# Performance work log

Measured on AMD Instinct MI355X. Metric: run time of the kernel, lower is better.

The kernel has to match this reference:

```python
import jax, jax.numpy as jnp
import numpy as np

B, L, C, H, FF = 2, 2048, 1024, 16, 4096
HD = C // H
SCALE = HD ** -0.5
EPS = 1e-5


def _ln(x, g, b):
    m = jnp.mean(x, axis=-1, keepdims=True)
    v = jnp.mean((x - m) ** 2, axis=-1, keepdims=True)
    return (x - m) * jax.lax.rsqrt(v + EPS) * g + b


def setup_inputs() -> dict:
    key = jax.random.key(0)
    ks = jax.random.split(key, 12)
    s = lambda fan_in: 1.0 / np.sqrt(fan_in)
    return {
        "x": jax.random.normal(ks[0], (B, L, C), jnp.float32),
        "freq_diff": jax.random.normal(ks[1], (B, L), jnp.float32),
        "qkv_w": jax.random.normal(ks[2], (C, 3 * C), jnp.float32) * s(C),
        "qkv_b": jnp.zeros((3 * C,), jnp.float32),
        "fp_w1": jax.random.normal(ks[3], (1, C), jnp.float32),
        "fp_b1": jnp.zeros((C,), jnp.float32),
        "fp_ln_g": jnp.ones((C,), jnp.float32),
        "fp_ln_b": jnp.zeros((C,), jnp.float32),
        "fp_w2": jax.random.normal(ks[4], (C, C), jnp.float32) * s(C),
        "fp_b2": jnp.zeros((C,), jnp.float32),
        "wq_w": jax.random.normal(ks[5], (HD, HD), jnp.float32) * s(HD),
        "wq_b": jnp.zeros((HD,), jnp.float32),
        "wk_w": jax.random.normal(ks[6], (HD, HD), jnp.float32) * s(HD),
        "wk_b": jnp.zeros((HD,), jnp.float32),
        "out_w": jax.random.normal(ks[7], (C, C), jnp.float32) * s(C),
        "out_b": jnp.zeros((C,), jnp.float32),
        "n1_g": jnp.ones((C,), jnp.float32),
        "n1_b": jnp.zeros((C,), jnp.float32),
        "n2_g": jnp.ones((C,), jnp.float32),
        "n2_b": jnp.zeros((C,), jnp.float32),
        "mlp_w1": jax.random.normal(ks[8], (C, FF), jnp.float32) * s(C),
        "mlp_b1": jnp.zeros((FF,), jnp.float32),
        "mlp_w2": jax.random.normal(ks[9], (FF, C), jnp.float32) * s(FF),
        "mlp_b2": jnp.zeros((C,), jnp.float32),
        "freq_scale": jnp.ones((1,), jnp.float32),
    }


def reference(x, freq_diff, qkv_w, qkv_b, fp_w1, fp_b1, fp_ln_g, fp_ln_b,
              fp_w2, fp_b2, wq_w, wq_b, wk_w, wk_b, out_w, out_b,
              n1_g, n1_b, n2_g, n2_b, mlp_w1, mlp_b1, mlp_w2, mlp_b2,
              freq_scale):
    shortcut = x
    xn = _ln(x, n1_g, n1_b)
    qkv = (xn @ qkv_w + qkv_b).reshape(B, L, 3, H, HD)
    qkv = jnp.transpose(qkv, (2, 0, 3, 1, 4))  # [3,B,H,L,HD]
    q, k, v = qkv[0], qkv[1], qkv[2]

    # frequency bias: MLP on scalar freq_diff -> per-head bias vectors
    fb = freq_diff[..., None] @ fp_w1 + fp_b1          # [B,L,C]
    fb = jax.nn.gelu(_ln(fb, fp_ln_g, fp_ln_b), approximate=False)
    fb = fb @ fp_w2 + fp_b2                            # [B,L,C]
    fb = jnp.transpose(fb.reshape(B, L, H, HD), (0, 2, 1, 3))  # [B,H,L,HD]
    qb = fb @ wq_w + wq_b
    kb = fb @ wk_w + wk_b
    freq_attn_bias = jnp.einsum('bhqd,bhkd->bhqk', qb, kb)

    attn = jnp.einsum('bhqd,bhkd->bhqk', q, k) * SCALE
    attn = attn + freq_scale[0] * freq_attn_bias
    attn = jax.nn.softmax(attn, axis=-1)
    o = jnp.einsum('bhqk,bhkd->bhqd', attn, v)
    o = jnp.transpose(o, (0, 2, 1, 3)).reshape(B, L, C)
    x = shortcut + (o @ out_w + out_b)

    xn2 = _ln(x, n2_g, n2_b)
    h = jax.nn.gelu(xn2 @ mlp_w1 + mlp_b1, approximate=False)
    x = x + (h @ mlp_w2 + mlp_b2)
    return x
```

## Files before the change

### kernel.cpp

```cpp
#include <hip/hip_runtime.h>
#include <math.h>


typedef __bf16 bf16;
typedef float f32x4 __attribute__((ext_vector_type(4)));
typedef bf16 bf16x8 __attribute__((ext_vector_type(8)));
typedef bf16 bf16x4 __attribute__((ext_vector_type(4)));

#define DEVINL __device__ __forceinline__

#define LOG2E 1.4426950408889634f

DEVINL float fast_exp2(float x) { return __builtin_amdgcn_exp2f(x); }

DEVINL void async_load16(const void* g, void* l) {
  __builtin_amdgcn_global_load_lds(
      (const __attribute__((address_space(1))) unsigned int*)g,
      (__attribute__((address_space(3))) unsigned int*)l, 16, 0, 0);
}

DEVINL f32x4 mfma16(bf16x8 a, bf16x8 b, f32x4 c) {
  return __builtin_amdgcn_mfma_f32_16x16x32_bf16(a, b, c, 0, 0, 0);
}

DEVINL float gelu_exact(float v) {
  return 0.5f * v * (1.0f + erff(v * 0.70710678118654752f));
}

DEVINL void hard_barrier() {
  asm volatile("" ::: "memory");
  __builtin_amdgcn_s_barrier();
  asm volatile("" ::: "memory");
}

DEVINL void block_reduce2(float& a, float& b, float* red, int tid) {
#pragma unroll
  for (int off = 32; off >= 1; off >>= 1) {
    a += __shfl_xor(a, off);
    b += __shfl_xor(b, off);
  }
  int w = tid >> 6;
  if ((tid & 63) == 0) { red[2 * w] = a; red[2 * w + 1] = b; }
  __syncthreads();
  a = red[0] + red[2] + red[4] + red[6];
  b = red[1] + red[3] + red[5] + red[7];
  __syncthreads();
}

__global__ __launch_bounds__(256) void pre_kernel(
    const float* __restrict__ qkv_w, const float* __restrict__ out_w,
    const float* __restrict__ mlp_w1, const float* __restrict__ mlp_w2,
    bf16* __restrict__ qkv_wt, bf16* __restrict__ out_wt,
    bf16* __restrict__ w1t, bf16* __restrict__ w2t,
    const float* __restrict__ x, const float* __restrict__ fd,
    const float* __restrict__ g1, const float* __restrict__ b1,
    const float* __restrict__ fw1, const float* __restrict__ fb1,
    const float* __restrict__ flg, const float* __restrict__ flb,
    bf16* __restrict__ xn, bf16* __restrict__ gout) {
  __shared__ float tile[32][33];
  __shared__ float red[8];
  const int id = blockIdx.x, t = threadIdx.x;
  if (id < 12288) {
    const float* W; bf16* Wt; int K, N, bx, by;
    if (id < 3072) {
      W = qkv_w; Wt = qkv_wt; K = 1024; N = 3072; bx = id % 96; by = id / 96;
    } else if (id < 4096) {
      int i = id - 3072;
      W = out_w; Wt = out_wt; K = 1024; N = 1024; bx = i & 31; by = i >> 5;
    } else if (id < 8192) {
      int i = id - 4096;
      W = mlp_w1; Wt = w1t; K = 1024; N = 4096; bx = i & 127; by = i >> 7;
    } else {
      int i = id - 8192;
      W = mlp_w2; Wt = w2t; K = 4096; N = 1024; bx = i & 31; by = i >> 5;
    }
    int n0 = bx * 32, k0 = by * 32;
    int tx = t & 31, ty = t >> 5;
#pragma unroll
    for (int r = 0; r < 4; ++r)
      tile[ty + r * 8][tx] = W[(size_t)(k0 + ty + r * 8) * N + n0 + tx];
    __syncthreads();
#pragma unroll
    for (int r = 0; r < 4; ++r)
      Wt[(size_t)(n0 + ty + r * 8) * K + k0 + tx] = (bf16)tile[tx][ty + r * 8];
    return;
  }
  int tok = id - 12288;
  float4 xv = ((const float4*)(x + (size_t)tok * 1024))[t];
  float s = xv.x + xv.y + xv.z + xv.w;
  float ss = xv.x * xv.x + xv.y * xv.y + xv.z * xv.z + xv.w * xv.w;
  block_reduce2(s, ss, red, t);
  float mean = s * (1.0f / 1024.0f);
  float rsig = rsqrtf(ss * (1.0f / 1024.0f) - mean * mean + 1e-5f);
  float4 g4 = ((const float4*)g1)[t], b4 = ((const float4*)b1)[t];
  bf16x4 o;
  o[0] = (bf16)((xv.x - mean) * rsig * g4.x + b4.x);
  o[1] = (bf16)((xv.y - mean) * rsig * g4.y + b4.y);
  o[2] = (bf16)((xv.z - mean) * rsig * g4.z + b4.z);
  o[3] = (bf16)((xv.w - mean) * rsig * g4.w + b4.w);
  ((bf16x4*)xn)[(size_t)tok * 256 + t] = o;

  float dv = fd[tok];
  float4 w4 = ((const float4*)fw1)[t], c4 = ((const float4*)fb1)[t];
  float f0 = dv * w4.x + c4.x, f1 = dv * w4.y + c4.y;
  float f2 = dv * w4.z + c4.z, f3 = dv * w4.w + c4.w;
  s = f0 + f1 + f2 + f3;
  ss = f0 * f0 + f1 * f1 + f2 * f2 + f3 * f3;
  block_reduce2(s, ss, red, t);
  mean = s * (1.0f / 1024.0f);
  rsig = rsqrtf(ss * (1.0f / 1024.0f) - mean * mean + 1e-5f);
  float4 lg = ((const float4*)flg)[t], lb = ((const float4*)flb)[t];
  bf16x4 q;
  q[0] = (bf16)gelu_exact((f0 - mean) * rsig * lg.x + lb.x);
  q[1] = (bf16)gelu_exact((f1 - mean) * rsig * lg.y + lb.y);
  q[2] = (bf16)gelu_exact((f2 - mean) * rsig * lg.z + lb.z);
  q[3] = (bf16)gelu_exact((f3 - mean) * rsig * lg.w + lb.w);
  ((bf16x4*)gout)[(size_t)tok * 256 + t] = q;
}

__global__ __launch_bounds__(256) void prec_qk(
    const float* __restrict__ fp_w2, const float* __restrict__ fp_b2,
    const float* __restrict__ wq_w, const float* __restrict__ wq_b,
    const float* __restrict__ wk_w, const float* __restrict__ wk_b,
    bf16* __restrict__ wqk2t, float* __restrict__ bqk) {
  __shared__ float Wl[64 * 64];
  __shared__ float Al[64 * 128];
  const int id = blockIdx.x;
  const int sel = id >> 7, h = (id >> 3) & 15, ck = id & 7;
  const int t = threadIdx.x;
  const float* wsel = sel ? wk_w : wq_w;
#pragma unroll
  for (int i = 0; i < 4; ++i)
    ((float4*)Wl)[i * 256 + t] = ((const float4*)wsel)[i * 256 + t];
  const int c0 = ck * 128, off = h * 64;
#pragma unroll
  for (int it = 0; it < 8; ++it) {
    int idx = it * 256 + t;
    int rr = idx >> 4, c4 = idx & 15;
    float4 v = *(const float4*)(fp_w2 + (size_t)(c0 + rr) * 1024 + off + c4 * 4);
    float vv[4] = {v.x, v.y, v.z, v.w};
#pragma unroll
    for (int k = 0; k < 4; ++k) {
      int i2 = c4 * 4 + k;
      Al[i2 * 128 + (rr ^ (i2 & 31))] = vv[k];
    }
  }
  __syncthreads();
  const int cr = t & 127, jh = (t >> 7) * 32;
  float acc[32];
#pragma unroll
  for (int j = 0; j < 32; ++j) acc[j] = 0.f;
  for (int i = 0; i < 64; ++i) {
    float a = Al[i * 128 + (cr ^ (i & 31))];
    const float4* wrow = (const float4*)(Wl + i * 64 + jh);
#pragma unroll
    for (int j4 = 0; j4 < 8; ++j4) {
      float4 wv = wrow[j4];
      acc[j4 * 4 + 0] += a * wv.x;
      acc[j4 * 4 + 1] += a * wv.y;
      acc[j4 * 4 + 2] += a * wv.z;
      acc[j4 * 4 + 3] += a * wv.w;
    }
  }
  const int nbase = sel * 1024 + off + jh;
#pragma unroll
  for (int j = 0; j < 32; ++j)
    wqk2t[(size_t)(nbase + j) * 1024 + c0 + cr] = (bf16)acc[j];
  if (ck == 0 && t < 64) {
    float s = 0.f;
    for (int i = 0; i < 64; ++i) s += fp_b2[off + i] * Wl[i * 64 + t];
    bqk[sel * 1024 + off + t] = s + (sel ? wk_b[t] : wq_b[t]);
  }
}

__global__ __launch_bounds__(256) void reduce_oln(
    const float* __restrict__ part, const float* __restrict__ x,
    const float* __restrict__ outb, const float* __restrict__ b2,
    const float* __restrict__ g, const float* __restrict__ bb,
    float* __restrict__ out0, bf16* __restrict__ ln2) {
  __shared__ float red[8];
  int tok = blockIdx.x, t = threadIdx.x;
  size_t base = (size_t)tok * 256 + t;
  const size_t S = (size_t)4096 * 256;
  float4 p0 = ((const float4*)part)[base];
  float4 p1 = ((const float4*)part)[base + S];
  float4 xv = ((const float4*)x)[base];
  float4 ob = ((const float4*)outb)[t];
  float v0 = xv.x + p0.x + p1.x + ob.x;
  float v1 = xv.y + p0.y + p1.y + ob.y;
  float v2 = xv.z + p0.z + p1.z + ob.z;
  float v3 = xv.w + p0.w + p1.w + ob.w;
  float s = v0 + v1 + v2 + v3;
  float ss = v0 * v0 + v1 * v1 + v2 * v2 + v3 * v3;
  block_reduce2(s, ss, red, t);
  float mean = s * (1.0f / 1024.0f);
  float rsig = rsqrtf(ss * (1.0f / 1024.0f) - mean * mean + 1e-5f);
  float4 g4 = ((const float4*)g)[t], bb4 = ((const float4*)bb)[t];
  bf16x4 o;
  o[0] = (bf16)((v0 - mean) * rsig * g4.x + bb4.x);
  o[1] = (bf16)((v1 - mean) * rsig * g4.y + bb4.y);
  o[2] = (bf16)((v2 - mean) * rsig * g4.z + bb4.z);
  o[3] = (bf16)((v3 - mean) * rsig * g4.w + bb4.w);
  ((bf16x4*)ln2)[base] = o;
  float4 b24 = ((const float4*)b2)[t];
  float4 ov;
  ov.x = v0 + b24.x; ov.y = v1 + b24.y; ov.z = v2 + b24.z; ov.w = v3 + b24.w;
  ((float4*)out0)[base] = ov;
}

#define PHASE(MH, NH, LA, LB, STAGE_STMT, WAIT_STMT)                          \
  do {                                                                        \
    if (LA) {                                                                 \
      _Pragma("unroll") for (int ml = 0; ml < 4; ++ml) {                      \
        _Pragma("unroll") for (int ks = 0; ks < 2; ++ks) {                    \
          const int rr = ml * 16 + lm;                                        \
          const int cc = (((ks * 4 + quad) ^ (lm & 7)) << 3);                 \
          af[ml][ks] = *(const bf16x8*)&As[bsel][MH][wm][rr][cc];             \
        }                                                                     \
      }                                                                       \
    }                                                                         \
    if (LB) {                                                                 \
      _Pragma("unroll") for (int nl = 0; nl < 2; ++nl) {                      \
        _Pragma("unroll") for (int ks = 0; ks < 2; ++ks) {                    \
          const int rr = nl * 16 + lm;                                        \
          const int cc = (((ks * 4 + quad) ^ (lm & 7)) << 3);                 \
          bfr[nl][ks] = *(const bf16x8*)&Bs[bsel][NH][wn][rr][cc];            \
        }                                                                     \
      }                                                                       \
    }                                                                         \
    STAGE_STMT;                                                               \
    WAIT_STMT;                                                                \
    hard_barrier();                                                           \
    __builtin_amdgcn_s_setprio(1);                                            \
    _Pragma("unroll") for (int ks = 0; ks < 2; ++ks) {                        \
      _Pragma("unroll") for (int ml = 0; ml < 4; ++ml) {                      \
        _Pragma("unroll") for (int nl = 0; nl < 2; ++nl) {                    \
          acc[(MH)*4 + ml][(NH)*2 + nl] = mfma16(                             \
              af[ml][ks], bfr[nl][ks], acc[(MH)*4 + ml][(NH)*2 + nl]);        \
        }                                                                     \
      }                                                                       \
    }                                                                         \
    __builtin_amdgcn_s_setprio(0);                                            \
  } while (0)

template <class Epi>
__global__ __launch_bounds__(512, 2) void gemm256(
    const bf16* __restrict__ A, const bf16* __restrict__ Bt,
    int lda, int ldb, int K, int kstride, int nbx, int nblk, int rowoffz,
    Epi epi) {
  __shared__ __align__(16) bf16 As[2][2][2][64][64];
  __shared__ __align__(16) bf16 Bs[2][2][4][32][64];

  const int tid = threadIdx.x;
  const int lane = tid & 63, w = tid >> 6;
  const int quad = lane >> 4, lm = lane & 15;
  const int wm = w >> 2, wn = w & 3;

  const int kz = blockIdx.x / nblk;
  const int bid = blockIdx.x - kz * nblk;
  const int swz = (nblk & 7) ? bid : ((bid & 7) * (nblk >> 3) + (bid >> 3));
  const int tm = swz / nbx, tn = swz - tm * nbx;
  const int m0 = tm << 8, n0 = tn << 8;
  const int rowoff = kz * rowoffz;
  A += (size_t)kz * kstride;
  Bt += (size_t)kz * kstride;

  const bf16* Abase = A + (size_t)m0 * lda;
  const bf16* Bbase = Bt + (size_t)n0 * ldb;

  auto stageA = [&](int b, int mh, int kt) {
#pragma unroll
    for (int j = 0; j < 2; ++j) {
      const int q = (w * 2 + j) * 64 + lane;
      const int wm2 = q >> 9, rr = (q >> 3) & 63, c = q & 7;
      async_load16(Abase + (size_t)(wm2 * 128 + mh * 64 + rr) * lda +
                       (size_t)kt * 64 + ((c ^ (rr & 7)) << 3),
                   (char*)&As[b][mh][0][0][0] + (w * 2 + j) * 1024);
    }
  };
  auto stageB = [&](int b, int nh, int kt) {
#pragma unroll
    for (int j = 0; j < 2; ++j) {
      const int q = (w * 2 + j) * 64 + lane;
      const int wn4 = q >> 8, rr = (q >> 3) & 31, c = q & 7;
      async_load16(Bbase + (size_t)(wn4 * 64 + nh * 32 + rr) * ldb +
                       (size_t)kt * 64 + ((c ^ (rr & 7)) << 3),
                   (char*)&Bs[b][nh][0][0][0] + (w * 2 + j) * 1024);
    }
  };

  f32x4 acc[8][4];
#pragma unroll
  for (int i = 0; i < 8; ++i)
#pragma unroll
    for (int j = 0; j < 4; ++j) {
      acc[i][j][0] = 0.f; acc[i][j][1] = 0.f;
      acc[i][j][2] = 0.f; acc[i][j][3] = 0.f;
    }
  bf16x8 af[4][2], bfr[2][2];

  stageA(0, 0, 0);
  stageB(0, 1, 0);
  stageA(0, 1, 0);
  stageB(0, 0, 0);
  stageA(1, 0, 1);
  stageB(1, 1, 1);
  asm volatile("s_waitcnt vmcnt(4)" ::: "memory");
  hard_barrier();

  const int nt = K >> 6;
  int bsel = 0;
  for (int t = 0; t < nt; ++t, bsel ^= 1) {
    PHASE(0, 0, 1, 1, { if (t + 1 < nt) stageA(bsel ^ 1, 1, t + 1); }, {});
    PHASE(0, 1, 0, 1, { if (t + 1 < nt) stageB(bsel ^ 1, 0, t + 1); }, {});
    PHASE(1, 1, 1, 0, { if (t + 2 < nt) stageA(bsel, 0, t + 2); }, {});
    PHASE(1, 0, 0, 1, { if (t + 2 < nt) stageB(bsel, 1, t + 2); },
          {
            if (t + 2 < nt) {
              asm volatile("s_waitcnt vmcnt(4)" ::: "memory");
            } else if (t + 1 < nt) {
              asm volatile("s_waitcnt vmcnt(0)" ::: "memory");
            }
          });
  }

#pragma unroll
  for (int mi = 0; mi < 8; ++mi)
#pragma unroll
    for (int ni = 0; ni < 4; ++ni)
      epi(rowoff + m0 + wm * 128 + mi * 16 + quad * 4,
          n0 + wn * 64 + ni * 16 + lm, acc[mi][ni]);
}

__global__ __launch_bounds__(256) void reduce_mlp2(
    const float* __restrict__ part, float* __restrict__ out) {
  size_t i = (size_t)blockIdx.x * 256 + threadIdx.x;
  const float4* p = (const float4*)part;
  float4 o = ((const float4*)out)[i];
  const size_t S = (size_t)4096 * 256;
  float4 a = p[i], b = p[i + S], c = p[i + 2 * S], d = p[i + 3 * S];
  o.x += a.x + b.x + c.x + d.x;
  o.y += a.y + b.y + c.y + d.y;
  o.z += a.z + b.z + c.z + d.z;
  o.w += a.w + b.w + c.w + d.w;
  ((float4*)out)[i] = o;
}

struct EpiQKV {
  const float* __restrict__ bias;
  bf16 *Qc, *Kc, *Vt;
  DEVINL void operator()(int row, int col, f32x4 v) const {
    int b = row >> 11, l = row & 2047;
    float bia = bias[col];
    if (col < 1024) {
      int h = col >> 6, d = col & 63;
      bf16* p = Qc + (size_t)(((b << 4) + h) * 2048 + l) * 128 + d;
#pragma unroll
      for (int r = 0; r < 4; ++r) p[r * 128] = (bf16)((v[r] + bia) * (0.125f * LOG2E));
    } else if (col < 2048) {
      int c2 = col - 1024, h = c2 >> 6, d = c2 & 63;
      bf16* p = Kc + (size_t)(((b << 4) + h) * 2048 + l) * 128 + d;
#pragma unroll
      for (int r = 0; r < 4; ++r) p[r * 128] = (bf16)(v[r] + bia);
    } else {
      int c2 = col - 2048, h = c2 >> 6, d = c2 & 63;
      bf16x4 pk;
#pragma unroll
      for (int r = 0; r < 4; ++r) pk[r] = (bf16)(v[r] + bia);
      *(bf16x4*)(Vt + (size_t)(((b << 4) + h) * 64 + d) * 2048 + l) = pk;
    }
  }
};

struct EpiQBKB {
  const float* __restrict__ bias;
  const float* __restrict__ fs;
  bf16 *Qc, *Kc;
  DEVINL void operator()(int row, int col, f32x4 v) const {
    int b = row >> 11, l = row & 2047;
    float bia = bias[col];
    if (col < 1024) {
      int h = col >> 6, d = col & 63;
      float sc = fs[0] * LOG2E;
      bf16* p = Qc + (size_t)(((b << 4) + h) * 2048 + l) * 128 + 64 + d;
#pragma unroll
      for (int r = 0; r < 4; ++r) p[r * 128] = (bf16)((v[r] + bia) * sc);
    } else {
      int c2 = col - 1024, h = c2 >> 6, d = c2 & 63;
      bf16* p = Kc + (size_t)(((b << 4) + h) * 2048 + l) * 128 + 64 + d;
#pragma unroll
      for (int r = 0; r < 4; ++r) p[r * 128] = (bf16)(v[r] + bia);
    }
  }
};

struct EpiMLP1 {
  const float* __restrict__ bias;
  bf16* hbf;
  DEVINL void operator()(int row, int col, f32x4 v) const {
    float bia = bias[col];
#pragma unroll
    for (int r = 0; r < 4; ++r)
      hbf[(size_t)(row + r) * 4096 + col] = (bf16)gelu_exact(v[r] + bia);
  }
};

struct EpiPart {
  float* part;
  DEVINL void operator()(int row, int col, f32x4 v) const {
#pragma unroll
    for (int r = 0; r < 4; ++r)
      part[(size_t)(row + r) * 1024 + col] = v[r];
  }
};

__global__ __launch_bounds__(512, 2) void flash_kernel(
    const bf16* __restrict__ Qc, const bf16* __restrict__ Kcp,
    const bf16* __restrict__ Vt, bf16* __restrict__ Obf) {
  __shared__ bf16 KsA[64 * 128];
  __shared__ bf16 KsB[64 * 128];
  __shared__ bf16 VsA[64 * 64];
  __shared__ bf16 VsB[64 * 64];
  __shared__ bf16 Ps[256 * 64];

  const int tid = threadIdx.x, lane = tid & 63, w = tid >> 6;
  const int quad = lane >> 4, lm = lane & 15;
  const int id = blockIdx.x;
  const int bh = id & 31, qt = id >> 5;
  const int b = bh >> 4, h = bh & 15;
  const int qrw = w * 32;

  const bf16* Kg0 = Kcp + (size_t)bh * 2048 * 128;
  const bf16* Vg0 = Vt + (size_t)bh * 64 * 2048;

  auto stage = [&](int kv, bf16* Kdst, bf16* Vdst) {
    const bf16* Kg = Kg0 + (size_t)kv * 64 * 128;
#pragma unroll
    for (int i = 0; i < 2; ++i) {
      int ch = i * 512 + tid, key = ch >> 4, c = (ch & 15) ^ (key & 7);
      async_load16(Kg + (size_t)key * 128 + c * 8,
                   (char*)Kdst + (i * 512 + w * 64) * 16);
    }
    {
      int d = tid >> 3, c = (tid & 7) ^ (d & 7);
      async_load16(Vg0 + (size_t)d * 2048 + kv * 64 + c * 8,
                   (char*)Vdst + (w * 64) * 16);
    }
  };

  stage(0, KsA, VsA);

  const bf16* Qg = Qc + ((size_t)bh * 2048 + qt * 256) * 128;
  bf16x8 qf[2][4];
#pragma unroll
  for (int qh = 0; qh < 2; ++qh)
#pragma unroll
    for (int ks = 0; ks < 4; ++ks)
      qf[qh][ks] = *(const bf16x8*)(Qg + (size_t)(qrw + qh * 16 + lm) * 128 +
                                    (ks * 4 + quad) * 8);

  float m_run[2] = {-3.0e38f, -3.0e38f};
  float l_lane[2] = {0.f, 0.f};
  f32x4 o_acc[2][4];
#pragma unroll
  for (int qh = 0; qh < 2; ++qh)
#pragma unroll
    for (int nf = 0; nf < 4; ++nf) {
      o_acc[qh][nf][0] = 0.f; o_acc[qh][nf][1] = 0.f;
      o_acc[qh][nf][2] = 0.f; o_acc[qh][nf][3] = 0.f;
    }

  for (int kv = 0; kv < 32; ++kv) {
    const bf16* Kcur = (kv & 1) ? KsB : KsA;
    const bf16* Vcur = (kv & 1) ? VsB : VsA;
    __syncthreads();
    if (kv + 1 < 32)
      stage(kv + 1, (kv & 1) ? KsA : KsB, (kv & 1) ? VsA : VsB);

    f32x4 sa[2][4];
#pragma unroll
    for (int qh = 0; qh < 2; ++qh)
#pragma unroll
      for (int nk = 0; nk < 4; ++nk) {
        sa[qh][nk][0] = 0.f; sa[qh][nk][1] = 0.f;
        sa[qh][nk][2] = 0.f; sa[qh][nk][3] = 0.f;
      }
#pragma unroll
    for (int ks = 0; ks < 4; ++ks) {
      bf16x8 ak[4];
#pragma unroll
      for (int nk = 0; nk < 4; ++nk) {
        int key = nk * 16 + lm;
        int pos = (ks * 4 + quad) ^ (key & 7);
        ak[nk] = *(const bf16x8*)(Kcur + key * 128 + pos * 8);
      }
#pragma unroll
      for (int nk = 0; nk < 4; ++nk) {
        sa[0][nk] = mfma16(ak[nk], qf[0][ks], sa[0][nk]);
        sa[1][nk] = mfma16(ak[nk], qf[1][ks], sa[1][nk]);
      }
    }

#pragma unroll
    for (int qh = 0; qh < 2; ++qh) {
      float mx = fmaxf(fmaxf(sa[qh][0][0], sa[qh][0][1]), sa[qh][0][2]);
      mx = fmaxf(fmaxf(mx, sa[qh][0][3]), sa[qh][1][0]);
      mx = fmaxf(fmaxf(mx, sa[qh][1][1]), sa[qh][1][2]);
      mx = fmaxf(fmaxf(mx, sa[qh][1][3]), sa[qh][2][0]);
      mx = fmaxf(fmaxf(mx, sa[qh][2][1]), sa[qh][2][2]);
      mx = fmaxf(fmaxf(mx, sa[qh][2][3]), sa[qh][3][0]);
      mx = fmaxf(fmaxf(mx, sa[qh][3][1]), sa[qh][3][2]);
      mx = fmaxf(mx, sa[qh][3][3]);
      mx = fmaxf(mx, __shfl_xor(mx, 16));
      mx = fmaxf(mx, __shfl_xor(mx, 32));
      if (__any(mx > m_run[qh] + 8.0f)) {
        float mnew = fmaxf(m_run[qh], mx);
        float alpha = fast_exp2(m_run[qh] - mnew);
        m_run[qh] = mnew;
        l_lane[qh] *= alpha;
#pragma unroll
        for (int nf = 0; nf < 4; ++nf) {
          o_acc[qh][nf][0] *= alpha; o_acc[qh][nf][1] *= alpha;
          o_acc[qh][nf][2] *= alpha; o_acc[qh][nf][3] *= alpha;
        }
      }
      float rs = 0.f;
#pragma unroll
      for (int nk = 0; nk < 4; ++nk)
#pragma unroll
        for (int rg = 0; rg < 4; ++rg) {
          float pv = fast_exp2(sa[qh][nk][rg] - m_run[qh]);
          sa[qh][nk][rg] = pv;
          rs += pv;
        }
      l_lane[qh] += rs;

      int qr = qrw + qh * 16 + lm;
#pragma unroll
      for (int nk = 0; nk < 4; ++nk) {
        int c16 = 2 * nk + (quad >> 1);
        int cs = c16 ^ (lm & 7);
        bf16x4 pk;
        pk[0] = (bf16)sa[qh][nk][0]; pk[1] = (bf16)sa[qh][nk][1];
        pk[2] = (bf16)sa[qh][nk][2]; pk[3] = (bf16)sa[qh][nk][3];
        *(bf16x4*)(Ps + qr * 64 + cs * 8 + (quad & 1) * 4) = pk;
      }
    }

#pragma unroll
    for (int ks = 0; ks < 2; ++ks) {
      bf16x8 vb[4], pa[2];
#pragma unroll
      for (int nf = 0; nf < 4; ++nf) {
        int d = nf * 16 + lm;
        int cs = (ks * 4 + quad) ^ (d & 7);
        vb[nf] = *(const bf16x8*)(Vcur + d * 64 + cs * 8);
      }
#pragma unroll
      for (int qh = 0; qh < 2; ++qh) {
        int qr = qrw + qh * 16 + lm;
        int cs = (ks * 4 + quad) ^ (lm & 7);
        pa[qh] = *(const bf16x8*)(Ps + qr * 64 + cs * 8);
      }
#pragma unroll
      for (int qh = 0; qh < 2; ++qh)
#pragma unroll
        for (int nf = 0; nf < 4; ++nf)
          o_acc[qh][nf] = mfma16(vb[nf], pa[qh], o_acc[qh][nf]);
    }
  }

#pragma unroll
  for (int qh = 0; qh < 2; ++qh) {
    float lt = l_lane[qh];
    lt += __shfl_xor(lt, 16);
    lt += __shfl_xor(lt, 32);
    float inv = 1.0f / lt;
    int l = qt * 256 + qrw + qh * 16 + lm;
#pragma unroll
    for (int nf = 0; nf < 4; ++nf) {
      bf16x4 ov;
#pragma unroll
      for (int rg = 0; rg < 4; ++rg) ov[rg] = (bf16)(o_acc[qh][nf][rg] * inv);
      int d = h * 64 + nf * 16 + quad * 4;
      *(bf16x4*)(Obf + ((size_t)b * 2048 + l) * 1024 + d) = ov;
    }
  }
}

extern "C" void kernel_launch(void* const* d_in, const int* in_sizes, int n_in,
                              void* d_out, int out_size, void* d_ws, size_t ws_size,
                              hipStream_t stream) {
  (void)in_sizes; (void)n_in; (void)out_size; (void)ws_size;
  const float* x      = (const float*)d_in[0];
  const float* fd     = (const float*)d_in[1];
  const float* qkv_w  = (const float*)d_in[2];
  const float* qkv_b  = (const float*)d_in[3];
  const float* fp_w1  = (const float*)d_in[4];
  const float* fp_b1  = (const float*)d_in[5];
  const float* fp_ln_g= (const float*)d_in[6];
  const float* fp_ln_b= (const float*)d_in[7];
  const float* fp_w2  = (const float*)d_in[8];
  const float* fp_b2  = (const float*)d_in[9];
  const float* wq_w   = (const float*)d_in[10];
  const float* wq_b   = (const float*)d_in[11];
  const float* wk_w   = (const float*)d_in[12];
  const float* wk_b   = (const float*)d_in[13];
  const float* out_w  = (const float*)d_in[14];
  const float* out_b  = (const float*)d_in[15];
  const float* n1_g   = (const float*)d_in[16];
  const float* n1_b   = (const float*)d_in[17];
  const float* n2_g   = (const float*)d_in[18];
  const float* n2_b   = (const float*)d_in[19];
  const float* mlp_w1 = (const float*)d_in[20];
  const float* mlp_b1 = (const float*)d_in[21];
  const float* mlp_w2 = (const float*)d_in[22];
  const float* mlp_b2 = (const float*)d_in[23];
  const float* fscale = (const float*)d_in[24];
  float* out = (float*)d_out;

  char* p = (char*)d_ws;
  auto take = [&](size_t n) { char* r = p; p += (n + 255) & ~(size_t)255; return r; };
  bf16* xn_bf  = (bf16*)take((size_t)4096 * 1024 * 2);
  bf16* g_bf   = (bf16*)take((size_t)4096 * 1024 * 2);
  bf16* Qc     = (bf16*)take((size_t)32 * 2048 * 128 * 2);
  bf16* Kc     = (bf16*)take((size_t)32 * 2048 * 128 * 2);
  bf16* Vt     = (bf16*)take((size_t)32 * 64 * 2048 * 2);
  bf16* o_bf   = (bf16*)take((size_t)4096 * 1024 * 2);
  bf16* ln2_bf = (bf16*)take((size_t)4096 * 1024 * 2);
  bf16* h_bf   = (bf16*)take((size_t)4096 * 4096 * 2);
  bf16* qkv_wt = (bf16*)take((size_t)3072 * 1024 * 2);
  bf16* out_wt = (bf16*)take((size_t)1024 * 1024 * 2);
  bf16* w1t    = (bf16*)take((size_t)4096 * 1024 * 2);
  bf16* w2t    = (bf16*)take((size_t)1024 * 4096 * 2);
  bf16* wqk2t  = (bf16*)take((size_t)2048 * 1024 * 2);
  float* bqk   = (float*)take((size_t)2048 * 4);

  float* part = (float*)xn_bf;
  float* opart = (float*)h_bf;

  dim3 b256(256), b512(512);

  prec_qk<<<dim3(256), b256, 0, stream>>>(fp_w2, fp_b2, wq_w, wq_b, wk_w, wk_b, wqk2t, bqk);
  pre_kernel<<<dim3(16384), b256, 0, stream>>>(
      qkv_w, out_w, mlp_w1, mlp_w2, qkv_wt, out_wt, w1t, w2t,
      x, fd, n1_g, n1_b, fp_w1, fp_b1, fp_ln_g, fp_ln_b, xn_bf, g_bf);

  gemm256<<<dim3(192), b512, 0, stream>>>(xn_bf, qkv_wt, 1024, 1024, 1024, 0,
                                          12, 192, 0, EpiQKV{qkv_b, Qc, Kc, Vt});
  gemm256<<<dim3(128), b512, 0, stream>>>(g_bf, wqk2t, 1024, 1024, 1024, 0,
                                          8, 128, 0, EpiQBKB{bqk, fscale, Qc, Kc});
  flash_kernel<<<dim3(256), dim3(512), 0, stream>>>(Qc, Kc, Vt, o_bf);

  gemm256<<<dim3(128), b512, 0, stream>>>(o_bf, out_wt, 1024, 1024, 512, 512,
                                          4, 64, 4096, EpiPart{opart});
  reduce_oln<<<dim3(4096), b256, 0, stream>>>(opart, x, out_b, mlp_b2,
                                              n2_g, n2_b, out, ln2_bf);
  gemm256<<<dim3(256), b512, 0, stream>>>(ln2_bf, w1t, 1024, 1024, 1024, 0,
                                          16, 256, 0, EpiMLP1{mlp_b1, h_bf});
  gemm256<<<dim3(256), b512, 0, stream>>>(h_bf, w2t, 4096, 4096, 1024, 1024,
                                          4, 64, 4096, EpiPart{part});
  reduce_mlp2<<<dim3(4096), b256, 0, stream>>>(part, out);
}
```

Measured before the change: 446.1 us.

## Fuse MLP2 split-K reduction via atomics, pad P tile, raise MFMA priority

The split-K partial buffer and the separate reduce kernel for the second MLP GEMM are removed. The GEMM epilogue now atomically adds each partial into the output, which already holds the residual. In the flash kernel, the P staging buffer row stride is padded from 64 to 80 elements to change LDS bank mapping. The MFMA sections are wrapped in s_setprio to favour matrix issue. The atomics cost contention on fp32 global adds and make the summation order nondeterministic, and the padded row stride increases LDS use.

```diff
diff --git a/kernel.cpp b/kernel.cpp
--- a/kernel.cpp
+++ b/kernel.cpp
@@ -332,20 +332,6 @@
           n0 + wn * 64 + ni * 16 + lm, acc[mi][ni]);
 }
 
-__global__ __launch_bounds__(256) void reduce_mlp2(
-    const float* __restrict__ part, float* __restrict__ out) {
-  size_t i = (size_t)blockIdx.x * 256 + threadIdx.x;
-  const float4* p = (const float4*)part;
-  float4 o = ((const float4*)out)[i];
-  const size_t S = (size_t)4096 * 256;
-  float4 a = p[i], b = p[i + S], c = p[i + 2 * S], d = p[i + 3 * S];
-  o.x += a.x + b.x + c.x + d.x;
-  o.y += a.y + b.y + c.y + d.y;
-  o.z += a.z + b.z + c.z + d.z;
-  o.w += a.w + b.w + c.w + d.w;
-  ((float4*)out)[i] = o;
-}
-
 struct EpiQKV {
   const float* __restrict__ bias;
   bf16 *Qc, *Kc, *Vt;
@@ -414,6 +400,17 @@
   }
 };
 
+struct EpiMLP2Atomic {
+  float* out;
+  DEVINL void operator()(int row, int col, f32x4 v) const {
+#pragma unroll
+    for (int r = 0; r < 4; ++r)
+      atomicAdd(out + (size_t)(row + r) * 1024 + col, v[r]);
+  }
+};
+
+#define PSS 80
+
 __global__ __launch_bounds__(512, 2) void flash_kernel(
     const bf16* __restrict__ Qc, const bf16* __restrict__ Kcp,
     const bf16* __restrict__ Vt, bf16* __restrict__ Obf) {
@@ -421,7 +418,7 @@
   __shared__ bf16 KsB[64 * 128];
   __shared__ bf16 VsA[64 * 64];
   __shared__ bf16 VsB[64 * 64];
-  __shared__ bf16 Ps[256 * 64];
+  __shared__ bf16 Ps[256 * PSS];
 
   const int tid = threadIdx.x, lane = tid & 63, w = tid >> 6;
   const int quad = lane >> 4, lm = lane & 15;
@@ -485,6 +482,7 @@
         sa[qh][nk][0] = 0.f; sa[qh][nk][1] = 0.f;
         sa[qh][nk][2] = 0.f; sa[qh][nk][3] = 0.f;
       }
+    __builtin_amdgcn_s_setprio(1);
 #pragma unroll
     for (int ks = 0; ks < 4; ++ks) {
       bf16x8 ak[4];
@@ -500,6 +498,7 @@
         sa[1][nk] = mfma16(ak[nk], qf[1][ks], sa[1][nk]);
       }
     }
+    __builtin_amdgcn_s_setprio(0);
 
 #pragma unroll
     for (int qh = 0; qh < 2; ++qh) {
@@ -543,7 +542,7 @@
         bf16x4 pk;
         pk[0] = (bf16)sa[qh][nk][0]; pk[1] = (bf16)sa[qh][nk][1];
         pk[2] = (bf16)sa[qh][nk][2]; pk[3] = (bf16)sa[qh][nk][3];
-        *(bf16x4*)(Ps + qr * 64 + cs * 8 + (quad & 1) * 4) = pk;
+        *(bf16x4*)(Ps + qr * PSS + cs * 8 + (quad & 1) * 4) = pk;
       }
     }
 
@@ -560,13 +559,15 @@
       for (int qh = 0; qh < 2; ++qh) {
         int qr = qrw + qh * 16 + lm;
         int cs = (ks * 4 + quad) ^ (lm & 7);
-        pa[qh] = *(const bf16x8*)(Ps + qr * 64 + cs * 8);
+        pa[qh] = *(const bf16x8*)(Ps + qr * PSS + cs * 8);
       }
+      __builtin_amdgcn_s_setprio(1);
 #pragma unroll
       for (int qh = 0; qh < 2; ++qh)
 #pragma unroll
         for (int nf = 0; nf < 4; ++nf)
           o_acc[qh][nf] = mfma16(vb[nf], pa[qh], o_acc[qh][nf]);
+      __builtin_amdgcn_s_setprio(0);
     }
   }
 
@@ -636,7 +637,6 @@
   bf16* wqk2t  = (bf16*)take((size_t)2048 * 1024 * 2);
   float* bqk   = (float*)take((size_t)2048 * 4);
 
-  float* part = (float*)xn_bf;
   float* opart = (float*)h_bf;
 
   dim3 b256(256), b512(512);
@@ -659,6 +659,5 @@
   gemm256<<<dim3(256), b512, 0, stream>>>(ln2_bf, w1t, 1024, 1024, 1024, 0,
                                           16, 256, 0, EpiMLP1{mlp_b1, h_bf});
   gemm256<<<dim3(256), b512, 0, stream>>>(h_bf, w2t, 4096, 4096, 1024, 1024,
-                                          4, 64, 4096, EpiPart{part});
-  reduce_mlp2<<<dim3(4096), b256, 0, stream>>>(part, out);
-}
+                                          4, 64, 0, EpiMLP2Atomic{out});
+}
```

After: 473.9 us. 1.06x slower.
